# Kernel optimization log

Measured on AMD Instinct MI355X. Metric: run time of the kernel, lower is better.

Reference implementation:

```python
import jax, jax.numpy as jnp
import numpy as np

NY, NU, NHIDDEN = 64, 32, 512
T, BATCH = 512, 256
DAMP = 0.99


def setup_inputs() -> dict:
    key = jax.random.key(0)
    ks = jax.random.split(key, 8)
    nh2 = NHIDDEN // 2
    theta = jax.random.uniform(ks[0], (nh2,)) * (jnp.pi / 2)
    lmbd_real = DAMP * jnp.cos(theta)
    lmbd_imag = DAMP * jnp.sin(theta)
    B = jax.random.normal(ks[1], (NHIDDEN, NU)) / np.sqrt(NU) * np.sqrt(1.0 - DAMP ** 2)
    W_y2x = jax.random.normal(ks[2], (NHIDDEN, NY)) / np.sqrt(NY)
    b_y2x = jnp.zeros((NHIDDEN,), jnp.float32)
    W_x2y = jax.random.normal(ks[3], (NY, NHIDDEN)) / np.sqrt(NHIDDEN)
    b_x2y = jnp.zeros((NY,), jnp.float32)
    y0 = jax.random.normal(ks[4], (BATCH, NY), jnp.float32)
    U = jax.random.normal(ks[5], (T, BATCH, NU), jnp.float32)
    return {"y0": y0, "U": U, "lmbd_real": lmbd_real, "lmbd_imag": lmbd_imag,
            "B": B, "W_y2x": W_y2x, "b_y2x": b_y2x, "W_x2y": W_x2y, "b_x2y": b_x2y}


def reference(y0, U, lmbd_real, lmbd_imag, B, W_y2x, b_y2x, W_x2y, b_x2y):
    # x_{k+1} = x_k @ A^T + B u_k, where A = [[diag(lr), -diag(li)], [diag(li), diag(lr)]]
    # i.e. an elementwise complex rotation of the paired state halves.
    nh2 = lmbd_real.shape[0]
    Bu = jnp.einsum('tbu,hu->tbh', U, B)          # [T, batch, Nhidden]
    x0 = y0 @ W_y2x.T + b_y2x                     # [batch, Nhidden]

    def step(x, bu):
        xr, xi = x[..., :nh2], x[..., nh2:]
        nr = lmbd_real * xr - lmbd_imag * xi
        ni = lmbd_imag * xr + lmbd_real * xi
        xn = jnp.concatenate([nr, ni], axis=-1) + bu
        return xn, xn

    _, Xs = jax.lax.scan(step, x0, Bu)            # [T, batch, Nhidden]
    X = jnp.concatenate([x0[None], Xs], axis=0)   # [T+1, batch, Nhidden]
    Y = X @ W_x2y.T + b_x2y                       # [T+1, batch, Ny]
    return Y
```

## Files before the change

kernel.cpp:

```cpp
#include <hip/hip_runtime.h>


constexpr int NY  = 64;
constexpr int NU  = 32;
constexpr int NH  = 512;
constexpr int NH2 = 256;
constexpr int TT  = 512;
constexpr int BB  = 256;
constexpr int KK  = 16;
constexpr int NSS = TT / KK;

constexpr int USP = 40;
constexpr int XSP = 544;
constexpr int BUP = 516;
constexpr int PSP = 20;

typedef __attribute__((ext_vector_type(4))) short sh4;
typedef __attribute__((ext_vector_type(8))) short sh8;
typedef __attribute__((ext_vector_type(4))) float f32x4;

#define MFMA16(a, b, c) __builtin_amdgcn_mfma_f32_16x16x32_bf16((a), (b), (c), 0, 0, 0)

static __device__ __forceinline__ unsigned short bfh(float x) {
    return (unsigned short)(__float_as_uint(x) >> 16);
}
static __device__ __forceinline__ float bf2f(unsigned short h) {
    return __uint_as_float(((unsigned)h) << 16);
}
static __device__ __forceinline__ void cvt4(const float4 f, sh4& vh, sh4& vl) {
    const float e[4] = { f.x, f.y, f.z, f.w };
#pragma unroll
    for (int j = 0; j < 4; ++j) {
        const unsigned short h = bfh(e[j]);
        vh[j] = (short)h;
        vl[j] = (short)bfh(e[j] - bf2f(h));
    }
}
static __device__ __forceinline__ unsigned cvtpk(float a, float b) {
    unsigned r;
    asm("v_cvt_pk_bf16_f32 %0, %1, %2" : "=v"(r) : "v"(a), "v"(b));
    return r;
}
static __device__ __forceinline__ void xs_store(unsigned* xh, unsigned* xl, int idx,
                                                float xr, float xi) {
    const unsigned hp = cvtpk(xr, xi);
    const float rr = __uint_as_float(hp << 16);
    const float ri = __uint_as_float(hp & 0xffff0000u);
    xh[idx] = hp;
    xl[idx] = cvtpk(xr - rr, xi - ri);
}
static __device__ __forceinline__ void bar_lds() {
    __builtin_amdgcn_sched_barrier(0);
    asm volatile("s_waitcnt lgkmcnt(0)" ::: "memory");
    __builtin_amdgcn_s_barrier();
    __builtin_amdgcn_sched_barrier(0);
}

__global__ __launch_bounds__(512, 2)
void lru_fused_kernel(const float* __restrict__ y0,
                      const float* __restrict__ U,
                      const float* __restrict__ lmr,
                      const float* __restrict__ lmi,
                      const float* __restrict__ Bmat,
                      const float* __restrict__ Wy2x,
                      const float* __restrict__ by2x,
                      const float* __restrict__ Wx2y,
                      const float* __restrict__ bx2y,
                      float* __restrict__ Y)
{
    const int b    = blockIdx.x;
    const int tid  = threadIdx.x;
    const int w    = tid >> 6;
    const int l    = tid & 63;
    const int lr16 = l & 15;
    const int lg   = l >> 4;

    __shared__ unsigned short us_h[2][64][USP], us_l[2][64][USP];
    __shared__ unsigned short xs_h[2][KK][XSP], xs_l[2][KK][XSP];
    __shared__ float          bu[KK][BUP];
    __shared__ float          psy[4][2][16][PSP];
    __shared__ float          y0s[NY];

    sh8 frg[32];
    float lamr = 0.f, lami = 0.f, xr = 0.f, xi = 0.f;
    float biasE = 0.f;
    int   xwrd  = 0;

    if (tid < NH2) {
#pragma unroll
        for (int q = 0; q < 8; ++q) {
            sh8 vh, vl;
#pragma unroll
            for (int h2 = 0; h2 < 2; ++h2) {
                const int hrow = (w << 7) + (q << 4) + lr16;
                const int u0   = (h2 << 4) + (lg << 2);
                const float4 f4 = *reinterpret_cast<const float4*>(&Bmat[hrow * NU + u0]);
                sh4 th, tl;
                cvt4(f4, th, tl);
#pragma unroll
                for (int j = 0; j < 4; ++j) { vh[h2 * 4 + j] = th[j]; vl[h2 * 4 + j] = tl[j]; }
            }
            frg[q] = vh;
            frg[8 + q] = vl;
        }
        lamr = lmr[tid];
        lami = lmi[tid];
        const int q_ = tid & 15, blk = tid >> 4;
        xwrd = blk * 16 + ((q_ & 7) >> 1) * 4 + (q_ >> 3) * 2 + (q_ & 1);
    } else {
        const int j = w - 4, ntp = j >> 1, kh = j & 1;
#pragma unroll
        for (int ntt = 0; ntt < 2; ++ntt) {
            const int n = ((ntp << 1) + ntt) * 16 + lr16;
            const float* Wn = Wx2y + n * NH;
#pragma unroll
            for (int ks = 0; ks < 8; ++ks) {
                sh8 vh, vl;
#pragma unroll
                for (int h2 = 0; h2 < 2; ++h2) {
                    const int k0 = (kh << 8) + (ks << 5) + (h2 << 4) + (lg << 2);
                    const int p0 = k0 >> 1;
                    const float e[4] = { Wn[p0], Wn[p0 + 256], Wn[p0 + 1], Wn[p0 + 257] };
#pragma unroll
                    for (int j2 = 0; j2 < 4; ++j2) {
                        const unsigned short h = bfh(e[j2]);
                        vh[h2 * 4 + j2] = (short)h;
                        vl[h2 * 4 + j2] = (short)bfh(e[j2] - bf2f(h));
                    }
                }
                frg[ntt * 8 + ks] = vh;
                frg[16 + ntt * 8 + ks] = vl;
            }
        }
        biasE = bx2y[(j << 4) + lr16];
    }

    const float4* Ug = reinterpret_cast<const float4*>(U);
    {
        const int i = tid, t = i >> 3, g = i & 7;
        const float4 f = Ug[((t * BB + b) << 3) + g];
        const int pos = (g < 4) ? (g << 3) : (((g - 4) << 3) + 4);
        sh4 vh, vl;
        cvt4(f, vh, vl);
        *reinterpret_cast<sh4*>(&us_h[0][t][pos]) = vh;
        *reinterpret_cast<sh4*>(&us_l[0][t][pos]) = vl;
    }
    if (tid < NY) y0s[tid] = y0[b * NY + tid];
    __syncthreads();

    if (tid < NH2) {
        const float* wr = &Wy2x[tid * NY];
        const float* wi = &Wy2x[(NH2 + tid) * NY];
        float a0 = 0, a1 = 0, a2 = 0, a3 = 0;
        float c0 = 0, c1 = 0, c2 = 0, c3 = 0;
#pragma unroll
        for (int y = 0; y < NY; y += 4) {
            a0 += wr[y + 0] * y0s[y + 0];
            a1 += wr[y + 1] * y0s[y + 1];
            a2 += wr[y + 2] * y0s[y + 2];
            a3 += wr[y + 3] * y0s[y + 3];
            c0 += wi[y + 0] * y0s[y + 0];
            c1 += wi[y + 1] * y0s[y + 1];
            c2 += wi[y + 2] * y0s[y + 2];
            c3 += wi[y + 3] * y0s[y + 3];
        }
        xr = by2x[tid]       + (a0 + a1) + (a2 + a3);
        xi = by2x[NH2 + tid] + (c0 + c1) + (c2 + c3);
        xs_store(reinterpret_cast<unsigned*>(&xs_h[1][0][0]),
                 reinterpret_cast<unsigned*>(&xs_l[1][0][0]), xwrd, xr, xi);
    }
    __syncthreads();

    float4 pf0, pf1;

    for (int st = 0; st <= NSS; ++st) {
        if (tid < NH2) {
            if (st < NSS) {
                const int su = (st >> 2) & 1, t0 = (st & 3) << 4;
                const sh8 auh = *reinterpret_cast<const sh8*>(&us_h[su][t0 + lr16][lg << 3]);
                const sh8 aul = *reinterpret_cast<const sh8*>(&us_l[su][t0 + lr16][lg << 3]);
#pragma unroll
                for (int q = 0; q < 8; ++q) {
                    f32x4 acc = (f32x4){0.f, 0.f, 0.f, 0.f};
                    acc = MFMA16(auh, frg[q], acc);
                    acc = MFMA16(aul, frg[q], acc);
                    acc = MFMA16(auh, frg[8 + q], acc);
                    const int h = (w << 7) + (q << 4) + lr16;
                    const int c = (h < NH2) ? (h << 1) : (((h - NH2) << 1) | 1);
#pragma unroll
                    for (int r = 0; r < 4; ++r)
                        bu[(lg << 2) + r][c] = acc[r];
                }
            }
        } else {
            const int cc = st >> 2;
            if ((st & 3) == 0 && cc < 7 && st < NSS) {
                const int i0 = tid - NH2, i1 = tid;
                pf0 = Ug[(((((cc + 1) << 6) + (i0 >> 3)) * BB + b) << 3) + (i0 & 7)];
                pf1 = Ug[(((((cc + 1) << 6) + (i1 >> 3)) * BB + b) << 3) + (i1 & 7)];
            }
            const int sx = (st + 1) & 1;
            const int j = w - 4, kh = j & 1;
            f32x4 a0a = (f32x4){0.f, 0.f, 0.f, 0.f};
            f32x4 a1a = (f32x4){0.f, 0.f, 0.f, 0.f};
            f32x4 a0b = (f32x4){0.f, 0.f, 0.f, 0.f};
            f32x4 a1b = (f32x4){0.f, 0.f, 0.f, 0.f};
#pragma unroll
            for (int ks = 0; ks < 4; ++ks) {
                const int sp = (kh << 8) + (ks << 5) + (lg << 3);
                const sh8 axh = *reinterpret_cast<const sh8*>(&xs_h[sx][lr16][sp]);
                const sh8 axl = *reinterpret_cast<const sh8*>(&xs_l[sx][lr16][sp]);
                a0a = MFMA16(axh, frg[ks], a0a);
                a0a = MFMA16(axl, frg[ks], a0a);
                a0a = MFMA16(axh, frg[16 + ks], a0a);
                a1a = MFMA16(axh, frg[8 + ks], a1a);
                a1a = MFMA16(axl, frg[8 + ks], a1a);
                a1a = MFMA16(axh, frg[24 + ks], a1a);
            }
#pragma unroll
            for (int ks = 4; ks < 8; ++ks) {
                const int sp = (kh << 8) + (ks << 5) + (lg << 3);
                const sh8 axh = *reinterpret_cast<const sh8*>(&xs_h[sx][lr16][sp]);
                const sh8 axl = *reinterpret_cast<const sh8*>(&xs_l[sx][lr16][sp]);
                a0b = MFMA16(axh, frg[ks], a0b);
                a0b = MFMA16(axl, frg[ks], a0b);
                a0b = MFMA16(axh, frg[16 + ks], a0b);
                a1b = MFMA16(axh, frg[8 + ks], a1b);
                a1b = MFMA16(axl, frg[8 + ks], a1b);
                a1b = MFMA16(axh, frg[24 + ks], a1b);
            }
            const f32x4 A0 = a0a + a0b;
            const f32x4 A1 = a1a + a1b;
#pragma unroll
            for (int r = 0; r < 4; ++r) {
                psy[j][0][(lg << 2) + r][lr16] = A0[r];
                psy[j][1][(lg << 2) + r][lr16] = A1[r];
            }
        }
        bar_lds();

        if (tid < NH2) {
            if (st < NSS) {
                const int sw = st & 1;
                unsigned* xh = reinterpret_cast<unsigned*>(&xs_h[sw][0][0]);
                unsigned* xl = reinterpret_cast<unsigned*>(&xs_l[sw][0][0]);
                float2 bu2[KK];
#pragma unroll
                for (int k = 0; k < KK; ++k)
                    bu2[k] = *reinterpret_cast<const float2*>(&bu[k][tid << 1]);
#pragma unroll
                for (int k = 0; k < KK; ++k) {
                    const float nr = lamr * xr - lami * xi + bu2[k].x;
                    const float ni = lami * xr + lamr * xi + bu2[k].y;
                    xr = nr;
                    xi = ni;
                    xs_store(xh, xl, k * (XSP / 2) + xwrd, xr, xi);
                }
            }
        } else {
            if ((st & 3) == 1 && (st >> 2) < 7) {
                const int ns = ((st >> 2) + 1) & 1;
#pragma unroll
                for (int v = 0; v < 2; ++v) {
                    const float4 f = v ? pf1 : pf0;
                    const int i = v ? tid : (tid - NH2);
                    const int t = i >> 3, g = i & 7;
                    const int pos = (g < 4) ? (g << 3) : (((g - 4) << 3) + 4);
                    sh4 vh, vl;
                    cvt4(f, vh, vl);
                    *reinterpret_cast<sh4*>(&us_h[ns][t][pos]) = vh;
                    *reinterpret_cast<sh4*>(&us_l[ns][t][pos]) = vl;
                }
            }
            const int j = w - 4;
            const int j0 = j & ~1;
#pragma unroll
            for (int r = 0; r < 4; ++r) {
                const int m = (lg << 2) + r;
                const float v = psy[j0][j & 1][m][lr16] + psy[j0 + 1][j & 1][m][lr16] + biasE;
                if (st == 0) {
                    if (m == 0) Y[b * NY + (j << 4) + lr16] = v;
                } else {
                    const int s = ((st - 1) << 4) + m + 1;
                    Y[(s * BB + b) * NY + (j << 4) + lr16] = v;
                }
            }
        }
        bar_lds();
    }
}

extern "C" void kernel_launch(void* const* d_in, const int* in_sizes, int n_in,
                              void* d_out, int out_size, void* d_ws, size_t ws_size,
                              hipStream_t stream) {
    const float* y0   = (const float*)d_in[0];
    const float* U    = (const float*)d_in[1];
    const float* lmr  = (const float*)d_in[2];
    const float* lmi  = (const float*)d_in[3];
    const float* Bm   = (const float*)d_in[4];
    const float* Wy2x = (const float*)d_in[5];
    const float* by2x = (const float*)d_in[6];
    const float* Wx2y = (const float*)d_in[7];
    const float* bx2y = (const float*)d_in[8];
    float* Y = (float*)d_out;

    lru_fused_kernel<<<dim3(BB), dim3(512), 0, stream>>>(
        y0, U, lmr, lmi, Bm, Wy2x, by2x, Wx2y, bx2y, Y);
}
```

Measured before the change: 165.0 us.

## Split recurrence into checkpoint pass plus time-chunked parallel output kernel

Replaces the single per-batch fused kernel with three launches. The first runs the recurrence without emitting outputs and saves the state every 64 steps to workspace. The second computes the initial output row, and the third launches 8 time chunks per batch (2048 blocks), each resuming from its checkpoint to recompute states and project them to Y. This exposes more blocks for parallelism and takes the output projection off the serial critical path, at the cost of running the Bu/state recurrence twice and adding extra launches and workspace traffic. The old monolithic kernel remains as a fallback when workspace is too small.

After: 311.7 us. +89.0%, slower.

```diff
diff --git a/kernel.cpp b/kernel.cpp
--- a/kernel.cpp
+++ b/kernel.cpp
@@ -5,15 +5,17 @@
 constexpr int NU  = 32;
 constexpr int NH  = 512;
 constexpr int NH2 = 256;
-constexpr int TT  = 512;
 constexpr int BB  = 256;
 constexpr int KK  = 16;
-constexpr int NSS = TT / KK;
-
+
+constexpr int MUSP = 40;
+constexpr int MXSP = 544;
+constexpr int MBUP = 516;
+constexpr int MPSP = 20;
 constexpr int USP = 40;
-constexpr int XSP = 544;
-constexpr int BUP = 516;
-constexpr int PSP = 20;
+constexpr int XSP = 520;
+constexpr int BUP = 513;
+constexpr int PSP = 74;
 
 typedef __attribute__((ext_vector_type(4))) short sh4;
 typedef __attribute__((ext_vector_type(8))) short sh8;
@@ -49,43 +51,22 @@
     xh[idx] = hp;
     xl[idx] = cvtpk(xr - rr, xi - ri);
 }
-static __device__ __forceinline__ void bar_lds() {
-    __builtin_amdgcn_sched_barrier(0);
-    asm volatile("s_waitcnt lgkmcnt(0)" ::: "memory");
-    __builtin_amdgcn_s_barrier();
-    __builtin_amdgcn_sched_barrier(0);
-}
 
 __global__ __launch_bounds__(512, 2)
-void lru_fused_kernel(const float* __restrict__ y0,
-                      const float* __restrict__ U,
-                      const float* __restrict__ lmr,
-                      const float* __restrict__ lmi,
-                      const float* __restrict__ Bmat,
-                      const float* __restrict__ Wy2x,
-                      const float* __restrict__ by2x,
-                      const float* __restrict__ Wx2y,
-                      const float* __restrict__ bx2y,
-                      float* __restrict__ Y)
+void k_state(const float* __restrict__ y0, const float* __restrict__ U,
+             const float* __restrict__ lmr, const float* __restrict__ lmi,
+             const float* __restrict__ Bmat, const float* __restrict__ Wy2x,
+             const float* __restrict__ by2x, float* __restrict__ wsX)
 {
-    const int b    = blockIdx.x;
-    const int tid  = threadIdx.x;
-    const int w    = tid >> 6;
-    const int l    = tid & 63;
-    const int lr16 = l & 15;
-    const int lg   = l >> 4;
-
-    __shared__ unsigned short us_h[2][64][USP], us_l[2][64][USP];
-    __shared__ unsigned short xs_h[2][KK][XSP], xs_l[2][KK][XSP];
-    __shared__ float          bu[KK][BUP];
-    __shared__ float          psy[4][2][16][PSP];
-    __shared__ float          y0s[NY];
-
-    sh8 frg[32];
+    const int b = blockIdx.x, tid = threadIdx.x;
+    const int w = tid >> 6, l = tid & 63, lr16 = l & 15, lg = l >> 4;
+
+    __shared__ unsigned short us_h[2][64][MUSP], us_l[2][64][MUSP];
+    __shared__ float bu[KK][MBUP];
+    __shared__ float y0s[NY];
+
+    sh8 fbh[8], fbl[8];
     float lamr = 0.f, lami = 0.f, xr = 0.f, xi = 0.f;
-    float biasE = 0.f;
-    int   xwrd  = 0;
-
     if (tid < NH2) {
 #pragma unroll
         for (int q = 0; q < 8; ++q) {
@@ -100,39 +81,11 @@
 #pragma unroll
                 for (int j = 0; j < 4; ++j) { vh[h2 * 4 + j] = th[j]; vl[h2 * 4 + j] = tl[j]; }
             }
-            frg[q] = vh;
-            frg[8 + q] = vl;
+            fbh[q] = vh;
+            fbl[q] = vl;
         }
         lamr = lmr[tid];
         lami = lmi[tid];
-        const int q_ = tid & 15, blk = tid >> 4;
-        xwrd = blk * 16 + ((q_ & 7) >> 1) * 4 + (q_ >> 3) * 2 + (q_ & 1);
-    } else {
-        const int j = w - 4, ntp = j >> 1, kh = j & 1;
-#pragma unroll
-        for (int ntt = 0; ntt < 2; ++ntt) {
-            const int n = ((ntp << 1) + ntt) * 16 + lr16;
-            const float* Wn = Wx2y + n * NH;
-#pragma unroll
-            for (int ks = 0; ks < 8; ++ks) {
-                sh8 vh, vl;
-#pragma unroll
-                for (int h2 = 0; h2 < 2; ++h2) {
-                    const int k0 = (kh << 8) + (ks << 5) + (h2 << 4) + (lg << 2);
-                    const int p0 = k0 >> 1;
-                    const float e[4] = { Wn[p0], Wn[p0 + 256], Wn[p0 + 1], Wn[p0 + 257] };
-#pragma unroll
-                    for (int j2 = 0; j2 < 4; ++j2) {
-                        const unsigned short h = bfh(e[j2]);
-                        vh[h2 * 4 + j2] = (short)h;
-                        vl[h2 * 4 + j2] = (short)bfh(e[j2] - bf2f(h));
-                    }
-                }
-                frg[ntt * 8 + ks] = vh;
-                frg[16 + ntt * 8 + ks] = vl;
-            }
-        }
-        biasE = bx2y[(j << 4) + lr16];
     }
 
     const float4* Ug = reinterpret_cast<const float4*>(U);
@@ -166,6 +119,368 @@
         }
         xr = by2x[tid]       + (a0 + a1) + (a2 + a3);
         xi = by2x[NH2 + tid] + (c0 + c1) + (c2 + c3);
+    }
+
+    float4 pf0, pf1;
+    for (int st = 0; st < 32; ++st) {
+        if (tid < NH2 && (st & 3) == 0) {
+            wsX[(b * 8 + (st >> 2)) * 512 + tid]       = xr;
+            wsX[(b * 8 + (st >> 2)) * 512 + 256 + tid] = xi;
+        }
+        if (tid < NH2) {
+            const int su = (st >> 2) & 1, t0 = (st & 3) << 4;
+            const sh8 auh = *reinterpret_cast<const sh8*>(&us_h[su][t0 + lr16][lg << 3]);
+            const sh8 aul = *reinterpret_cast<const sh8*>(&us_l[su][t0 + lr16][lg << 3]);
+#pragma unroll
+            for (int q = 0; q < 8; ++q) {
+                f32x4 acc = (f32x4){0.f, 0.f, 0.f, 0.f};
+                acc = MFMA16(auh, fbh[q], acc);
+                acc = MFMA16(aul, fbh[q], acc);
+                acc = MFMA16(auh, fbl[q], acc);
+                const int h = (w << 7) + (q << 4) + lr16;
+#pragma unroll
+                for (int r = 0; r < 4; ++r) bu[(lg << 2) + r][h] = acc[r];
+            }
+        } else {
+            const int cc = st >> 2;
+            if ((st & 3) == 0 && cc < 7) {
+                const int i0 = tid - NH2, i1 = tid;
+                pf0 = Ug[(((((cc + 1) << 6) + (i0 >> 3)) * BB + b) << 3) + (i0 & 7)];
+                pf1 = Ug[(((((cc + 1) << 6) + (i1 >> 3)) * BB + b) << 3) + (i1 & 7)];
+            }
+        }
+        __syncthreads();
+        if (tid < NH2) {
+#pragma unroll
+            for (int k = 0; k < KK; ++k) {
+                const float bur = bu[k][tid];
+                const float bui = bu[k][256 + tid];
+                const float nr = lamr * xr - lami * xi + bur;
+                const float ni = lami * xr + lamr * xi + bui;
+                xr = nr;
+                xi = ni;
+            }
+        } else if ((st & 3) == 1 && (st >> 2) < 7) {
+            const int ns = ((st >> 2) + 1) & 1;
+#pragma unroll
+            for (int v = 0; v < 2; ++v) {
+                const float4 f = v ? pf1 : pf0;
+                const int i = v ? tid : (tid - NH2);
+                const int t = i >> 3, g = i & 7;
+                const int pos = (g < 4) ? (g << 3) : (((g - 4) << 3) + 4);
+                sh4 vh, vl;
+                cvt4(f, vh, vl);
+                *reinterpret_cast<sh4*>(&us_h[ns][t][pos]) = vh;
+                *reinterpret_cast<sh4*>(&us_l[ns][t][pos]) = vl;
+            }
+        }
+        __syncthreads();
+    }
+}
+
+__global__ __launch_bounds__(256)
+void k_y0(const float* __restrict__ Wx2y, const float* __restrict__ bx2y,
+          const float* __restrict__ wsX, float* __restrict__ Y)
+{
+    const int b = blockIdx.x, tid = threadIdx.x;
+    __shared__ float x0s[NH];
+    __shared__ float ps0[4][80];
+
+    x0s[tid]       = wsX[(b * 8) * 512 + tid];
+    x0s[256 + tid] = wsX[(b * 8) * 512 + 256 + tid];
+    __syncthreads();
+
+    const int n = tid & 63, kq = tid >> 6;
+    const float* Wn = Wx2y + n * NH + (kq << 7);
+    const float* xq = x0s + (kq << 7);
+    float a0 = 0, a1 = 0, a2 = 0, a3 = 0;
+#pragma unroll
+    for (int h = 0; h < 128; h += 4) {
+        a0 += Wn[h + 0] * xq[h + 0];
+        a1 += Wn[h + 1] * xq[h + 1];
+        a2 += Wn[h + 2] * xq[h + 2];
+        a3 += Wn[h + 3] * xq[h + 3];
+    }
+    ps0[kq][n] = (a0 + a1) + (a2 + a3);
+    __syncthreads();
+    if (tid < NY)
+        Y[b * NY + tid] = ps0[0][tid] + ps0[1][tid] + ps0[2][tid] + ps0[3][tid] + bx2y[tid];
+}
+
+__global__ __launch_bounds__(512, 4)
+void k_main(const float* __restrict__ U,
+            const float* __restrict__ lmr, const float* __restrict__ lmi,
+            const float* __restrict__ Bmat, const float* __restrict__ Wx2y,
+            const float* __restrict__ bx2y, const float* __restrict__ wsX,
+            float* __restrict__ Y)
+{
+    const int bc = blockIdx.x;
+    const int b = bc >> 3, c = bc & 7;
+    const int tid = threadIdx.x;
+    const int w = tid >> 6, l = tid & 63, lr16 = l & 15, lg = l >> 4;
+
+    __shared__ unsigned short us_h[KK][USP], us_l[KK][USP];
+    __shared__ unsigned short xs_h[KK][XSP], xs_l[KK][XSP];
+    __shared__ float bu[KK][BUP];
+    __shared__ float psy[2][KK][PSP];
+
+    sh8 bbh[4], bbl[4];
+#pragma unroll
+    for (int q = 0; q < 4; ++q) {
+        sh8 vh, vl;
+#pragma unroll
+        for (int h2 = 0; h2 < 2; ++h2) {
+            const int hrow = (w << 6) + (q << 4) + lr16;
+            const int u0   = (h2 << 4) + (lg << 2);
+            const float4 f4 = *reinterpret_cast<const float4*>(&Bmat[hrow * NU + u0]);
+            sh4 th, tl;
+            cvt4(f4, th, tl);
+#pragma unroll
+            for (int j = 0; j < 4; ++j) { vh[h2 * 4 + j] = th[j]; vl[h2 * 4 + j] = tl[j]; }
+        }
+        bbh[q] = vh;
+        bbl[q] = vl;
+    }
+
+    const int nt = w >> 1, kh = w & 1;
+    sh8 whi[8], wlo[8];
+    {
+        const float* Wn = Wx2y + ((nt << 4) + lr16) * NH;
+#pragma unroll
+        for (int ks = 0; ks < 8; ++ks) {
+            sh8 vh, vl;
+#pragma unroll
+            for (int h2 = 0; h2 < 2; ++h2) {
+                const int k0 = (kh << 8) + (ks << 5) + (h2 << 4) + (lg << 2);
+                const int p0 = k0 >> 1;
+                const float e[4] = { Wn[p0], Wn[p0 + 256], Wn[p0 + 1], Wn[p0 + 257] };
+#pragma unroll
+                for (int j2 = 0; j2 < 4; ++j2) {
+                    const unsigned short h = bfh(e[j2]);
+                    vh[h2 * 4 + j2] = (short)h;
+                    vl[h2 * 4 + j2] = (short)bfh(e[j2] - bf2f(h));
+                }
+            }
+            whi[ks] = vh;
+            wlo[ks] = vl;
+        }
+    }
+    const float bias = bx2y[l];
+
+    float lamr = 0.f, lami = 0.f, xr = 0.f, xi = 0.f;
+    int xwrd = 0;
+    if (tid < NH2) {
+        lamr = lmr[tid];
+        lami = lmi[tid];
+        xr = wsX[(b * 8 + c) * 512 + tid];
+        xi = wsX[(b * 8 + c) * 512 + 256 + tid];
+        const int q_ = tid & 15, blk = tid >> 4;
+        xwrd = blk * 16 + ((q_ & 7) >> 1) * 4 + (q_ >> 3) * 2 + (q_ & 1);
+    }
+
+    const float4* Ug = reinterpret_cast<const float4*>(U);
+    float4 pf;
+    if (tid < 128) {
+        const int tg = (c << 6) + (tid >> 3), g = tid & 7;
+        pf = Ug[(tg * BB + b) * 8 + g];
+    }
+
+    for (int ss = 0; ss < 4; ++ss) {
+        if (tid < 128) {
+            const float4 cur = pf;
+            if (ss < 3) {
+                const int tg = (c << 6) + ((ss + 1) << 4) + (tid >> 3), g = tid & 7;
+                pf = Ug[(tg * BB + b) * 8 + g];
+            }
+            const int t = tid >> 3, g = tid & 7;
+            const int pos = (g < 4) ? (g << 3) : (((g - 4) << 3) + 4);
+            sh4 vh, vl;
+            cvt4(cur, vh, vl);
+            *reinterpret_cast<sh4*>(&us_h[t][pos]) = vh;
+            *reinterpret_cast<sh4*>(&us_l[t][pos]) = vl;
+        }
+        if (ss > 0) {
+#pragma unroll
+            for (int rr = 0; rr < 2; ++rr) {
+                const int m = (w << 1) + rr;
+                const float v = psy[0][m][18 * lg + lr16] + psy[1][m][18 * lg + lr16] + bias;
+                const int s = (c << 6) + ((ss - 1) << 4) + m + 1;
+                Y[(s * BB + b) * NY + l] = v;
+            }
+        }
+        __syncthreads();
+        {
+            const sh8 auh = *reinterpret_cast<const sh8*>(&us_h[lr16][lg << 3]);
+            const sh8 aul = *reinterpret_cast<const sh8*>(&us_l[lr16][lg << 3]);
+#pragma unroll
+            for (int q = 0; q < 4; ++q) {
+                f32x4 acc = (f32x4){0.f, 0.f, 0.f, 0.f};
+                acc = MFMA16(auh, bbh[q], acc);
+                acc = MFMA16(aul, bbh[q], acc);
+                acc = MFMA16(auh, bbl[q], acc);
+                const int h = (w << 6) + (q << 4) + lr16;
+#pragma unroll
+                for (int r = 0; r < 4; ++r) bu[(lg << 2) + r][h] = acc[r];
+            }
+        }
+        __syncthreads();
+        if (tid < NH2) {
+            unsigned* xh = reinterpret_cast<unsigned*>(&xs_h[0][0]);
+            unsigned* xl = reinterpret_cast<unsigned*>(&xs_l[0][0]);
+#pragma unroll
+            for (int k = 0; k < KK; ++k) {
+                const float bur = bu[k][tid];
+                const float bui = bu[k][256 + tid];
+                const float nr = lamr * xr - lami * xi + bur;
+                const float ni = lami * xr + lamr * xi + bui;
+                xr = nr;
+                xi = ni;
+                xs_store(xh, xl, k * (XSP / 2) + xwrd, xr, xi);
+            }
+        }
+        __syncthreads();
+        {
+            f32x4 aa = (f32x4){0.f, 0.f, 0.f, 0.f};
+            f32x4 ab = (f32x4){0.f, 0.f, 0.f, 0.f};
+#pragma unroll
+            for (int ks = 0; ks < 4; ++ks) {
+                const int sp = (kh << 8) + (ks << 5) + (lg << 3);
+                const sh8 axh = *reinterpret_cast<const sh8*>(&xs_h[lr16][sp]);
+                const sh8 axl = *reinterpret_cast<const sh8*>(&xs_l[lr16][sp]);
+                aa = MFMA16(axh, whi[ks], aa);
+                aa = MFMA16(axl, whi[ks], aa);
+                aa = MFMA16(axh, wlo[ks], aa);
+            }
+#pragma unroll
+            for (int ks = 4; ks < 8; ++ks) {
+                const int sp = (kh << 8) + (ks << 5) + (lg << 3);
+                const sh8 axh = *reinterpret_cast<const sh8*>(&xs_h[lr16][sp]);
+                const sh8 axl = *reinterpret_cast<const sh8*>(&xs_l[lr16][sp]);
+                ab = MFMA16(axh, whi[ks], ab);
+                ab = MFMA16(axl, whi[ks], ab);
+                ab = MFMA16(axh, wlo[ks], ab);
+            }
+            const f32x4 A = aa + ab;
+#pragma unroll
+            for (int r = 0; r < 4; ++r)
+                psy[kh][(lg << 2) + r][18 * nt + lr16] = A[r];
+        }
+        __syncthreads();
+    }
+#pragma unroll
+    for (int rr = 0; rr < 2; ++rr) {
+        const int m = (w << 1) + rr;
+        const float v = psy[0][m][18 * lg + lr16] + psy[1][m][18 * lg + lr16] + bias;
+        const int s = (c << 6) + (3 << 4) + m + 1;
+        Y[(s * BB + b) * NY + l] = v;
+    }
+}
+
+__global__ __launch_bounds__(512, 2)
+void lru_mono(const float* __restrict__ y0, const float* __restrict__ U,
+              const float* __restrict__ lmr, const float* __restrict__ lmi,
+              const float* __restrict__ Bmat, const float* __restrict__ Wy2x,
+              const float* __restrict__ by2x, const float* __restrict__ Wx2y,
+              const float* __restrict__ bx2y, float* __restrict__ Y)
+{
+    const int b    = blockIdx.x;
+    const int tid  = threadIdx.x;
+    const int w    = tid >> 6;
+    const int l    = tid & 63;
+    const int lr16 = l & 15;
+    const int lg   = l >> 4;
+
+    __shared__ unsigned short us_h[2][64][MUSP], us_l[2][64][MUSP];
+    __shared__ unsigned short xs_h[2][KK][MXSP], xs_l[2][KK][MXSP];
+    __shared__ float          bu[KK][MBUP];
+    __shared__ float          psy[4][2][16][MPSP];
+    __shared__ float          y0s[NY];
+
+    sh8 frg[32];
+    float lamr = 0.f, lami = 0.f, xr = 0.f, xi = 0.f;
+    float biasE = 0.f;
+    int   xwrd  = 0;
+
+    if (tid < NH2) {
+#pragma unroll
+        for (int q = 0; q < 8; ++q) {
+            sh8 vh, vl;
+#pragma unroll
+            for (int h2 = 0; h2 < 2; ++h2) {
+                const int hrow = (w << 7) + (q << 4) + lr16;
+                const int u0   = (h2 << 4) + (lg << 2);
+                const float4 f4 = *reinterpret_cast<const float4*>(&Bmat[hrow * NU + u0]);
+                sh4 th, tl;
+                cvt4(f4, th, tl);
+#pragma unroll
+                for (int j = 0; j < 4; ++j) { vh[h2 * 4 + j] = th[j]; vl[h2 * 4 + j] = tl[j]; }
+            }
+            frg[q] = vh;
+            frg[8 + q] = vl;
+        }
+        lamr = lmr[tid];
+        lami = lmi[tid];
+        const int q_ = tid & 15, blk = tid >> 4;
+        xwrd = blk * 16 + ((q_ & 7) >> 1) * 4 + (q_ >> 3) * 2 + (q_ & 1);
+    } else {
+        const int j = w - 4, ntp = j >> 1, kh = j & 1;
+#pragma unroll
+        for (int ntt = 0; ntt < 2; ++ntt) {
+            const int n = ((ntp << 1) + ntt) * 16 + lr16;
+            const float* Wn = Wx2y + n * NH;
+#pragma unroll
+            for (int ks = 0; ks < 8; ++ks) {
+                sh8 vh, vl;
+#pragma unroll
+                for (int h2 = 0; h2 < 2; ++h2) {
+                    const int k0 = (kh << 8) + (ks << 5) + (h2 << 4) + (lg << 2);
+                    const int p0 = k0 >> 1;
+                    const float e[4] = { Wn[p0], Wn[p0 + 256], Wn[p0 + 1], Wn[p0 + 257] };
+#pragma unroll
+                    for (int j2 = 0; j2 < 4; ++j2) {
+                        const unsigned short h = bfh(e[j2]);
+                        vh[h2 * 4 + j2] = (short)h;
+                        vl[h2 * 4 + j2] = (short)bfh(e[j2] - bf2f(h));
+                    }
+                }
+                frg[ntt * 8 + ks] = vh;
+                frg[16 + ntt * 8 + ks] = vl;
+            }
+        }
+        biasE = bx2y[(j << 4) + lr16];
+    }
+
+    const float4* Ug = reinterpret_cast<const float4*>(U);
+    {
+        const int i = tid, t = i >> 3, g = i & 7;
+        const float4 f = Ug[((t * BB + b) << 3) + g];
+        const int pos = (g < 4) ? (g << 3) : (((g - 4) << 3) + 4);
+        sh4 vh, vl;
+        cvt4(f, vh, vl);
+        *reinterpret_cast<sh4*>(&us_h[0][t][pos]) = vh;
+        *reinterpret_cast<sh4*>(&us_l[0][t][pos]) = vl;
+    }
+    if (tid < NY) y0s[tid] = y0[b * NY + tid];
+    __syncthreads();
+
+    if (tid < NH2) {
+        const float* wr = &Wy2x[tid * NY];
+        const float* wi = &Wy2x[(NH2 + tid) * NY];
+        float a0 = 0, a1 = 0, a2 = 0, a3 = 0;
+        float c0 = 0, c1 = 0, c2 = 0, c3 = 0;
+#pragma unroll
+        for (int y = 0; y < NY; y += 4) {
+            a0 += wr[y + 0] * y0s[y + 0];
+            a1 += wr[y + 1] * y0s[y + 1];
+            a2 += wr[y + 2] * y0s[y + 2];
+            a3 += wr[y + 3] * y0s[y + 3];
+            c0 += wi[y + 0] * y0s[y + 0];
+            c1 += wi[y + 1] * y0s[y + 1];
+            c2 += wi[y + 2] * y0s[y + 2];
+            c3 += wi[y + 3] * y0s[y + 3];
+        }
+        xr = by2x[tid]       + (a0 + a1) + (a2 + a3);
+        xi = by2x[NH2 + tid] + (c0 + c1) + (c2 + c3);
         xs_store(reinterpret_cast<unsigned*>(&xs_h[1][0][0]),
                  reinterpret_cast<unsigned*>(&xs_l[1][0][0]), xwrd, xr, xi);
     }
@@ -173,9 +488,9 @@
 
     float4 pf0, pf1;
 
-    for (int st = 0; st <= NSS; ++st) {
+    for (int st = 0; st <= 32; ++st) {
         if (tid < NH2) {
-            if (st < NSS) {
+            if (st < 32) {
                 const int su = (st >> 2) & 1, t0 = (st & 3) << 4;
                 const sh8 auh = *reinterpret_cast<const sh8*>(&us_h[su][t0 + lr16][lg << 3]);
                 const sh8 aul = *reinterpret_cast<const sh8*>(&us_l[su][t0 + lr16][lg << 3]);
@@ -186,15 +501,13 @@
                     acc = MFMA16(aul, frg[q], acc);
                     acc = MFMA16(auh, frg[8 + q], acc);
                     const int h = (w << 7) + (q << 4) + lr16;
-                    const int c = (h < NH2) ? (h << 1) : (((h - NH2) << 1) | 1);
-#pragma unroll
-                    for (int r = 0; r < 4; ++r)
-                        bu[(lg << 2) + r][c] = acc[r];
+#pragma unroll
+                    for (int r = 0; r < 4; ++r) bu[(lg << 2) + r][h] = acc[r];
                 }
             }
         } else {
             const int cc = st >> 2;
-            if ((st & 3) == 0 && cc < 7 && st < NSS) {
+            if ((st & 3) == 0 && cc < 7 && st < 32) {
                 const int i0 = tid - NH2, i1 = tid;
                 pf0 = Ug[(((((cc + 1) << 6) + (i0 >> 3)) * BB + b) << 3) + (i0 & 7)];
                 pf1 = Ug[(((((cc + 1) << 6) + (i1 >> 3)) * BB + b) << 3) + (i1 & 7)];
@@ -203,10 +516,8 @@
             const int j = w - 4, kh = j & 1;
             f32x4 a0a = (f32x4){0.f, 0.f, 0.f, 0.f};
             f32x4 a1a = (f32x4){0.f, 0.f, 0.f, 0.f};
-            f32x4 a0b = (f32x4){0.f, 0.f, 0.f, 0.f};
-            f32x4 a1b = (f32x4){0.f, 0.f, 0.f, 0.f};
-#pragma unroll
-            for (int ks = 0; ks < 4; ++ks) {
+#pragma unroll
+            for (int ks = 0; ks < 8; ++ks) {
                 const int sp = (kh << 8) + (ks << 5) + (lg << 3);
                 const sh8 axh = *reinterpret_cast<const sh8*>(&xs_h[sx][lr16][sp]);
                 const sh8 axl = *reinterpret_cast<const sh8*>(&xs_l[sx][lr16][sp]);
@@ -218,43 +529,27 @@
                 a1a = MFMA16(axh, frg[24 + ks], a1a);
             }
 #pragma unroll
-            for (int ks = 4; ks < 8; ++ks) {
-                const int sp = (kh << 8) + (ks << 5) + (lg << 3);
-                const sh8 axh = *reinterpret_cast<const sh8*>(&xs_h[sx][lr16][sp]);
-                const sh8 axl = *reinterpret_cast<const sh8*>(&xs_l[sx][lr16][sp]);
-                a0b = MFMA16(axh, frg[ks], a0b);
-                a0b = MFMA16(axl, frg[ks], a0b);
-                a0b = MFMA16(axh, frg[16 + ks], a0b);
-                a1b = MFMA16(axh, frg[8 + ks], a1b);
-                a1b = MFMA16(axl, frg[8 + ks], a1b);
-                a1b = MFMA16(axh, frg[24 + ks], a1b);
-            }
-            const f32x4 A0 = a0a + a0b;
-            const f32x4 A1 = a1a + a1b;
-#pragma unroll
             for (int r = 0; r < 4; ++r) {
-                psy[j][0][(lg << 2) + r][lr16] = A0[r];
-                psy[j][1][(lg << 2) + r][lr16] = A1[r];
-            }
-        }
-        bar_lds();
+                psy[j][0][(lg << 2) + r][lr16] = a0a[r];
+                psy[j][1][(lg << 2) + r][lr16] = a1a[r];
+            }
+        }
+        __syncthreads();
 
         if (tid < NH2) {
-            if (st < NSS) {
+            if (st < 32) {
                 const int sw = st & 1;
                 unsigned* xh = reinterpret_cast<unsigned*>(&xs_h[sw][0][0]);
                 unsigned* xl = reinterpret_cast<unsigned*>(&xs_l[sw][0][0]);
-                float2 bu2[KK];
-#pragma unroll
-                for (int k = 0; k < KK; ++k)
-                    bu2[k] = *reinterpret_cast<const float2*>(&bu[k][tid << 1]);
 #pragma unroll
                 for (int k = 0; k < KK; ++k) {
-                    const float nr = lamr * xr - lami * xi + bu2[k].x;
-                    const float ni = lami * xr + lamr * xi + bu2[k].y;
+                    const float bur = bu[k][tid];
+                    const float bui = bu[k][256 + tid];
+                    const float nr = lamr * xr - lami * xi + bur;
+                    const float ni = lami * xr + lamr * xi + bui;
                     xr = nr;
                     xi = ni;
-                    xs_store(xh, xl, k * (XSP / 2) + xwrd, xr, xi);
+                    xs_store(xh, xl, k * (MXSP / 2) + xwrd, xr, xi);
                 }
             }
         } else {
@@ -286,7 +581,7 @@
                 }
             }
         }
-        bar_lds();
+        __syncthreads();
     }
 }
 
@@ -304,6 +599,14 @@
     const float* bx2y = (const float*)d_in[8];
     float* Y = (float*)d_out;
 
-    lru_fused_kernel<<<dim3(BB), dim3(512), 0, stream>>>(
-        y0, U, lmr, lmi, Bm, Wy2x, by2x, Wx2y, bx2y, Y);
-}
+    const size_t need = (size_t)256 * 8 * 512 * sizeof(float);
+    if (d_ws != nullptr && ws_size >= need) {
+        float* wsX = (float*)d_ws;
+        k_state<<<dim3(BB),   dim3(512), 0, stream>>>(y0, U, lmr, lmi, Bm, Wy2x, by2x, wsX);
+        k_y0   <<<dim3(BB),   dim3(256), 0, stream>>>(Wx2y, bx2y, wsX, Y);
+        k_main <<<dim3(2048), dim3(512), 0, stream>>>(U, lmr, lmi, Bm, Wx2y, bx2y, wsX, Y);
+    } else {
+        lru_mono<<<dim3(BB), dim3(512), 0, stream>>>(
+            y0, U, lmr, lmi, Bm, Wy2x, by2x, Wx2y, bx2y, Y);
+    }
+}
```
